# Kernel tuning notes

Hardware: AMD Instinct MI355X
Metric: run time of the kernel (lower is better)

## Reference

```python
import jax, jax.numpy as jnp
import numpy as np

B, C, H, W = 8, 64, 128, 128


def setup_inputs() -> dict:
    key = jax.random.key(0)
    k1, k2 = jax.random.split(key)
    x = jax.random.normal(k1, (B, C, H, W), dtype=jnp.float32)
    mask = jnp.ones((B, C, H, W), dtype=jnp.float32)
    v = jax.random.normal(k2, (B, C, H, W), dtype=jnp.float32)
    m = 0  # selects the argmax-scatter branch of Later_inhibt.forward
    return {"x": x, "mask": mask, "v": v, "m": m}


def reference(x, mask, v, m):
    # Faithful to the torch m==0 branch:
    #   index = argmax(v, dim=1)                      -> [B, H, W]
    #   mask_temp[:, index[0, i, j], i, j] = 1        (only batch-0 indices used,
    #                                                  written across all batches)
    #   mask = mask * mask_temp; mask = mask * x; return (x, mask)
    if m == 0:
        idx0 = jnp.argmax(v, axis=1)[0]                      # [H, W]
        onehot = jax.nn.one_hot(idx0, v.shape[1], dtype=x.dtype)  # [H, W, C]
        mask_temp = jnp.transpose(onehot, (2, 0, 1))[None]   # [1, C, H, W] -> broadcasts over B
        new_mask = mask * mask_temp * x                      # [B, C, H, W]
        return (x, new_mask)
    else:
        # m != 0 branch: zero spatial positions where channel-sum of (x + mask) > 1
        mask_temp = x  # self.mask is all-ones -> self.mask * x == x
        result = jnp.sum(mask_temp + mask, axis=1, keepdims=True)   # [B, 1, H, W]
        # torch zeroes flagged (h, w) positions across ALL batches/channels
        keep = ~jnp.any(result > 1, axis=(0, 1))                    # [H, W]
        mask_temp = mask_temp * keep[None, None, :, :].astype(x.dtype)
        new_mask = mask + mask_temp
        return (new_mask * x, new_mask)
```

## Files before the change

### kernel.cpp

```cpp
#include <hip/hip_runtime.h>

#define BB 8
#define CC 64
#define HW 16384
#define NTOT (BB * CC * HW)

__device__ int g_idx[HW];

__global__ void __launch_bounds__(256)
argmax_c_kernel(const float* __restrict__ v) {
    int pos = blockIdx.x * blockDim.x + threadIdx.x;
    float best = v[pos];
    int bi = 0;
#pragma unroll
    for (int c = 1; c < CC; ++c) {
        float val = v[c * HW + pos];
        if (val > best) { best = val; bi = c; }
    }
    g_idx[pos] = bi;
}

__global__ void __launch_bounds__(256)
onehot_mask_kernel(const float* __restrict__ x,
                   const float* __restrict__ mask,
                   float* __restrict__ out0,
                   float* __restrict__ out1) {
    int t = blockIdx.x * blockDim.x + threadIdx.x;
    int base = t << 2;
    if (base >= NTOT) return;

    const float4 x4 = *reinterpret_cast<const float4*>(x + base);

    int hw = base & (HW - 1);
    int c  = (base >> 14) & (CC - 1);
    const int4 i4 = *reinterpret_cast<const int4*>(g_idx + hw);

    *reinterpret_cast<float4*>(out0 + base) = x4;

    float4 o;
    o.x = (c == i4.x) ? mask[base + 0] * x4.x : 0.0f;
    o.y = (c == i4.y) ? mask[base + 1] * x4.y : 0.0f;
    o.z = (c == i4.z) ? mask[base + 2] * x4.z : 0.0f;
    o.w = (c == i4.w) ? mask[base + 3] * x4.w : 0.0f;
    *reinterpret_cast<float4*>(out1 + base) = o;
}

extern "C" void kernel_launch(void* const* d_in, const int* in_sizes, int n_in,
                              void* d_out, int out_size, void* d_ws, size_t ws_size,
                              hipStream_t stream) {
    const float* x    = (const float*)d_in[0];
    const float* mask = (const float*)d_in[1];
    const float* v    = (const float*)d_in[2];

    float* out0 = (float*)d_out;
    float* out1 = out0 + NTOT;

    argmax_c_kernel<<<HW / 256, 256, 0, stream>>>(v);

    onehot_mask_kernel<<<(NTOT / 4) / 256, 256, 0, stream>>>(x, mask, out0, out1);
}
```

Measured before the change: 140.3 us.

## Fuse channel argmax and one-hot masking into a single per-position-tile kernel

Merges the argmax kernel and the masking kernel into one launch. Each block owns 32 spatial positions: it computes the channel argmax in shared memory with a two-stage reduction across 8 channel groups, then streams all 512 batch-channel planes for those positions. This removes the second launch and the global index buffer. In exchange, each warp's accesses become 128-byte segments scattered across planes instead of fully contiguous streams, and the grid shrinks to 512 blocks, which may reduce memory-level parallelism.

```diff
diff --git a/kernel.cpp b/kernel.cpp
--- a/kernel.cpp
+++ b/kernel.cpp
@@ -3,46 +3,72 @@
 #define BB 8
 #define CC 64
 #define HW 16384
-#define NTOT (BB * CC * HW)
-
-__device__ int g_idx[HW];
+#define NPLANES (BB * CC)
+#define POS 32
+#define NBLK (HW / POS)
 
 __global__ void __launch_bounds__(256)
-argmax_c_kernel(const float* __restrict__ v) {
-    int pos = blockIdx.x * blockDim.x + threadIdx.x;
-    float best = v[pos];
-    int bi = 0;
+later_inhibt_fused(const float* __restrict__ x,
+                   const float* __restrict__ mask,
+                   const float* __restrict__ v,
+                   float* __restrict__ out0,
+                   float* __restrict__ out1)
+{
+    __shared__ float s_val[8][POS];
+    __shared__ int   s_idx[8][POS];
+    __shared__ int   s_win[POS];
+
+    const int t    = threadIdx.x;
+    const int pos0 = blockIdx.x * POS;
+
+    {
+        const int p  = t & (POS - 1);
+        const int cg = t >> 5;
+        const float* vp = v + pos0 + p;
+        const int c0 = cg * 8;
+        float best = vp[c0 * HW];
+        int   bi   = c0;
 #pragma unroll
-    for (int c = 1; c < CC; ++c) {
-        float val = v[c * HW + pos];
-        if (val > best) { best = val; bi = c; }
+        for (int k = 1; k < 8; ++k) {
+            float val = vp[(c0 + k) * HW];
+            if (val > best) { best = val; bi = c0 + k; }
+        }
+        s_val[cg][p] = best;
+        s_idx[cg][p] = bi;
     }
-    g_idx[pos] = bi;
-}
+    __syncthreads();
+    if (t < POS) {
+        float b = s_val[0][t];
+        int   w = s_idx[0][t];
+#pragma unroll
+        for (int g = 1; g < 8; ++g) {
+            if (s_val[g][t] > b) { b = s_val[g][t]; w = s_idx[g][t]; }
+        }
+        s_win[t] = w;
+    }
+    __syncthreads();
 
-__global__ void __launch_bounds__(256)
-onehot_mask_kernel(const float* __restrict__ x,
-                   const float* __restrict__ mask,
-                   float* __restrict__ out0,
-                   float* __restrict__ out1) {
-    int t = blockIdx.x * blockDim.x + threadIdx.x;
-    int base = t << 2;
-    if (base >= NTOT) return;
+    const int j    = t & 7;
+    const int prow = t >> 3;
+    const int4 w4  = *reinterpret_cast<const int4*>(&s_win[j * 4]);
+    const int  eo  = pos0 + j * 4;
 
-    const float4 x4 = *reinterpret_cast<const float4*>(x + base);
+#pragma unroll 4
+    for (int it = 0; it < NPLANES / 32; ++it) {
+        const int plane = it * 32 + prow;
+        const int c     = plane & (CC - 1);
+        const int base  = plane * HW + eo;
 
-    int hw = base & (HW - 1);
-    int c  = (base >> 14) & (CC - 1);
-    const int4 i4 = *reinterpret_cast<const int4*>(g_idx + hw);
+        const float4 x4 = *reinterpret_cast<const float4*>(x + base);
+        *reinterpret_cast<float4*>(out0 + base) = x4;
 
-    *reinterpret_cast<float4*>(out0 + base) = x4;
-
-    float4 o;
-    o.x = (c == i4.x) ? mask[base + 0] * x4.x : 0.0f;
-    o.y = (c == i4.y) ? mask[base + 1] * x4.y : 0.0f;
-    o.z = (c == i4.z) ? mask[base + 2] * x4.z : 0.0f;
-    o.w = (c == i4.w) ? mask[base + 3] * x4.w : 0.0f;
-    *reinterpret_cast<float4*>(out1 + base) = o;
+        float4 o;
+        o.x = (c == w4.x) ? mask[base + 0] * x4.x : 0.0f;
+        o.y = (c == w4.y) ? mask[base + 1] * x4.y : 0.0f;
+        o.z = (c == w4.z) ? mask[base + 2] * x4.z : 0.0f;
+        o.w = (c == w4.w) ? mask[base + 3] * x4.w : 0.0f;
+        *reinterpret_cast<float4*>(out1 + base) = o;
+    }
 }
 
 extern "C" void kernel_launch(void* const* d_in, const int* in_sizes, int n_in,
@@ -53,9 +79,7 @@
     const float* v    = (const float*)d_in[2];
 
     float* out0 = (float*)d_out;
-    float* out1 = out0 + NTOT;
+    float* out1 = out0 + (NPLANES * HW);
 
-    argmax_c_kernel<<<HW / 256, 256, 0, stream>>>(v);
-
-    onehot_mask_kernel<<<(NTOT / 4) / 256, 256, 0, stream>>>(x, mask, out0, out1);
+    later_inhibt_fused<<<NBLK, 256, 0, stream>>>(x, mask, v, out0, out1);
 }
```

Result: slower. 164.1 us (+17.0%).

## Split channel argmax across four thread groups and use vector loads with nontemporal stores

Applied to the files above, without the earlier changes.

The argmax kernel now splits the 64 channels into four groups of 16, one per 64-thread slice, and reduces the partial results through shared memory. This gives four times as many blocks, raising parallelism and memory-level concurrency for the small argmax pass. The mask kernel loads mask as one vector instead of four scalar loads and writes both outputs with nontemporal stores to reduce cache pollution. Ties still resolve to the lowest channel index. The trade-off is an extra barrier and shared-memory traffic in the argmax.

```diff
diff --git a/kernel.cpp b/kernel.cpp
--- a/kernel.cpp
+++ b/kernel.cpp
@@ -5,19 +5,42 @@
 #define HW 16384
 #define NTOT (BB * CC * HW)
 
+typedef float v4f __attribute__((ext_vector_type(4)));
+typedef int   v4i __attribute__((ext_vector_type(4)));
+
 __device__ int g_idx[HW];
 
 __global__ void __launch_bounds__(256)
 argmax_c_kernel(const float* __restrict__ v) {
-    int pos = blockIdx.x * blockDim.x + threadIdx.x;
-    float best = v[pos];
-    int bi = 0;
+    __shared__ float s_val[4][64];
+    __shared__ int   s_idx[4][64];
+
+    const int p   = threadIdx.x & 63;
+    const int g   = threadIdx.x >> 6;
+    const int pos = blockIdx.x * 64 + p;
+    const int c0  = g * 16;
+
+    const float* vp = v + pos;
+    float best = vp[c0 * HW];
+    int   bi   = c0;
 #pragma unroll
-    for (int c = 1; c < CC; ++c) {
-        float val = v[c * HW + pos];
-        if (val > best) { best = val; bi = c; }
+    for (int k = 1; k < 16; ++k) {
+        float val = vp[(c0 + k) * HW];
+        if (val > best) { best = val; bi = c0 + k; }
     }
-    g_idx[pos] = bi;
+    s_val[g][p] = best;
+    s_idx[g][p] = bi;
+    __syncthreads();
+
+    if (threadIdx.x < 64) {
+        float b = s_val[0][p];
+        int   w = s_idx[0][p];
+#pragma unroll
+        for (int q = 1; q < 4; ++q) {
+            if (s_val[q][p] > b) { b = s_val[q][p]; w = s_idx[q][p]; }
+        }
+        g_idx[pos] = w;
+    }
 }
 
 __global__ void __launch_bounds__(256)
@@ -25,24 +48,24 @@
                    const float* __restrict__ mask,
                    float* __restrict__ out0,
                    float* __restrict__ out1) {
-    int t = blockIdx.x * blockDim.x + threadIdx.x;
-    int base = t << 2;
-    if (base >= NTOT) return;
+    const int t    = blockIdx.x * blockDim.x + threadIdx.x;
+    const int base = t << 2;
 
-    const float4 x4 = *reinterpret_cast<const float4*>(x + base);
+    const v4f x4 = *reinterpret_cast<const v4f*>(x + base);
+    const v4f m4 = *reinterpret_cast<const v4f*>(mask + base);
 
-    int hw = base & (HW - 1);
-    int c  = (base >> 14) & (CC - 1);
-    const int4 i4 = *reinterpret_cast<const int4*>(g_idx + hw);
+    const int hw = base & (HW - 1);
+    const int c  = (base >> 14) & (CC - 1);
+    const v4i i4 = *reinterpret_cast<const v4i*>(g_idx + hw);
 
-    *reinterpret_cast<float4*>(out0 + base) = x4;
+    __builtin_nontemporal_store(x4, reinterpret_cast<v4f*>(out0 + base));
 
-    float4 o;
-    o.x = (c == i4.x) ? mask[base + 0] * x4.x : 0.0f;
-    o.y = (c == i4.y) ? mask[base + 1] * x4.y : 0.0f;
-    o.z = (c == i4.z) ? mask[base + 2] * x4.z : 0.0f;
-    o.w = (c == i4.w) ? mask[base + 3] * x4.w : 0.0f;
-    *reinterpret_cast<float4*>(out1 + base) = o;
+    v4f o;
+    o.x = (c == i4.x) ? m4.x * x4.x : 0.0f;
+    o.y = (c == i4.y) ? m4.y * x4.y : 0.0f;
+    o.z = (c == i4.z) ? m4.z * x4.z : 0.0f;
+    o.w = (c == i4.w) ? m4.w * x4.w : 0.0f;
+    __builtin_nontemporal_store(o, reinterpret_cast<v4f*>(out1 + base));
 }
 
 extern "C" void kernel_launch(void* const* d_in, const int* in_sizes, int n_in,
@@ -55,7 +78,6 @@
     float* out0 = (float*)d_out;
     float* out1 = out0 + NTOT;
 
-    argmax_c_kernel<<<HW / 256, 256, 0, stream>>>(v);
-
+    argmax_c_kernel<<<HW / 64, 256, 0, stream>>>(v);
     onehot_mask_kernel<<<(NTOT / 4) / 256, 256, 0, stream>>>(x, mask, out0, out1);
 }
```

New measurement: 141.5 us. No clear change (+0.9%).
